# Optimization experiments

Measured on AMD Instinct MI355X. Metric: run time of the kernel, lower is better.

The kernel has to match this reference:

```python
import jax, jax.numpy as jnp
import numpy as np
from jax import lax

EPS = 1e-5
B, CIN, H, W = 4, 512, 64, 64
CI = CIN // 4          # inter_channels = 128
CQK = CI // 8          # PAM query/key channels = 16
NC = 19                # num_classes


def conv2d(x, w, pad):
    return lax.conv_general_dilated(x, w, (1, 1), [(pad, pad), (pad, pad)],
                                    dimension_numbers=('NCHW', 'OIHW', 'NCHW'))


def bn_relu(x, g, b, m, v):
    # eval-mode BatchNorm2d followed by ReLU
    inv = g * lax.rsqrt(v + EPS)
    return jax.nn.relu(x * inv[None, :, None, None] + (b - m * inv)[None, :, None, None])


def setup_inputs() -> dict:
    key = jax.random.key(0)
    ks = iter(jax.random.split(key, 40))
    rn = lambda shape, s=0.02: (jax.random.normal(next(ks), shape, dtype=jnp.float32) * s)
    ones = lambda n: jnp.ones((n,), jnp.float32)
    zeros = lambda n: jnp.zeros((n,), jnp.float32)
    inp = {
        'x': jax.random.normal(next(ks), (B, CIN, H, W), dtype=jnp.float32),
        # conv_p1: 3x3 conv (no bias) + BN
        'wp1': rn((CI, CIN, 3, 3)),
        'bnp1_w': ones(CI), 'bnp1_b': zeros(CI), 'bnp1_m': zeros(CI), 'bnp1_v': ones(CI),
        # PAM 1x1 convs
        'qw': rn((CQK, CI, 1, 1)), 'qb': zeros(CQK),
        'kw': rn((CQK, CI, 1, 1)), 'kb': zeros(CQK),
        'vw': rn((CI, CI, 1, 1)), 'vb': zeros(CI),
        'pam_gamma': jnp.full((1,), 0.5, jnp.float32),
        # conv_p2
        'wp2': rn((CI, CI, 3, 3)),
        'bnp2_w': ones(CI), 'bnp2_b': zeros(CI), 'bnp2_m': zeros(CI), 'bnp2_v': ones(CI),
        # conv_c1
        'wc1': rn((CI, CIN, 3, 3)),
        'bnc1_w': ones(CI), 'bnc1_b': zeros(CI), 'bnc1_m': zeros(CI), 'bnc1_v': ones(CI),
        'cam_gamma': jnp.full((1,), 0.5, jnp.float32),
        # conv_c2
        'wc2': rn((CI, CI, 3, 3)),
        'bnc2_w': ones(CI), 'bnc2_b': zeros(CI), 'bnc2_m': zeros(CI), 'bnc2_v': ones(CI),
        # classifier heads (dropout is eval-mode identity)
        'cls_w': rn((NC, CI, 1, 1)), 'cls_b': zeros(NC),
        'auxp_w': rn((NC, CI, 1, 1)), 'auxp_b': zeros(NC),
        'auxc_w': rn((NC, CI, 1, 1)), 'auxc_b': zeros(NC),
    }
    return inp


def pam(x, qw, qb, kw, kb, vw, vb, gamma):
    b, c, h, w = x.shape
    n = h * w
    q = (conv2d(x, qw, 0) + qb[None, :, None, None]).reshape(b, -1, n)  # [B,CQK,N]
    k = (conv2d(x, kw, 0) + kb[None, :, None, None]).reshape(b, -1, n)  # [B,CQK,N]
    v = (conv2d(x, vw, 0) + vb[None, :, None, None]).reshape(b, c, n)   # [B,C,N]
    attn = jax.nn.softmax(jnp.einsum('bcn,bcm->bnm', q, k), axis=-1)    # [B,N,N]
    out = jnp.einsum('bcm,bnm->bcn', v, attn).reshape(b, c, h, w)
    return gamma * out + x


def cam(x, gamma):
    b, c, h, w = x.shape
    f = x.reshape(b, c, -1)                                             # [B,C,N]
    attn = jax.nn.softmax(jnp.einsum('bin,bjn->bij', f, f), axis=-1)    # [B,C,C]
    out = jnp.einsum('bij,bjn->bin', attn, f).reshape(b, c, h, w)
    return gamma * out + x


def _forward(x, wp1, bnp1_w, bnp1_b, bnp1_m, bnp1_v,
             qw, qb, kw, kb, vw, vb, pam_gamma,
             wp2, bnp2_w, bnp2_b, bnp2_m, bnp2_v,
             wc1, bnc1_w, bnc1_b, bnc1_m, bnc1_v, cam_gamma,
             wc2, bnc2_w, bnc2_b, bnc2_m, bnc2_v,
             cls_w, cls_b, auxp_w, auxp_b, auxc_w, auxc_b):
    feat_p = bn_relu(conv2d(x, wp1, 1), bnp1_w, bnp1_b, bnp1_m, bnp1_v)
    feat_p = pam(feat_p, qw, qb, kw, kb, vw, vb, pam_gamma)
    feat_p = bn_relu(conv2d(feat_p, wp2, 1), bnp2_w, bnp2_b, bnp2_m, bnp2_v)

    feat_c = bn_relu(conv2d(x, wc1, 1), bnc1_w, bnc1_b, bnc1_m, bnc1_v)
    feat_c = cam(feat_c, cam_gamma)
    feat_c = bn_relu(conv2d(feat_c, wc2, 1), bnc2_w, bnc2_b, bnc2_m, bnc2_v)

    feat = feat_p + feat_c
    out = conv2d(feat, cls_w, 0) + cls_b[None, :, None, None]
    out_p = conv2d(feat_p, auxp_w, 0) + auxp_b[None, :, None, None]
    out_c = conv2d(feat_c, auxc_w, 0) + auxc_b[None, :, None, None]
    return out, out_p, out_c


def reference(x, wp1, bnp1_w, bnp1_b, bnp1_m, bnp1_v,
              qw, qb, kw, kb, vw, vb, pam_gamma,
              wp2, bnp2_w, bnp2_b, bnp2_m, bnp2_v,
              wc1, bnc1_w, bnc1_b, bnc1_m, bnc1_v, cam_gamma,
              wc2, bnc2_w, bnc2_b, bnc2_m, bnc2_v,
              cls_w, cls_b, auxp_w, auxp_b, auxc_w, auxc_b):
    return _forward(x, wp1, bnp1_w, bnp1_b, bnp1_m, bnp1_v,
                    qw, qb, kw, kb, vw, vb, pam_gamma,
                    wp2, bnp2_w, bnp2_b, bnp2_m, bnp2_v,
                    wc1, bnc1_w, bnc1_b, bnc1_m, bnc1_v, cam_gamma,
                    wc2, bnc2_w, bnc2_b, bnc2_m, bnc2_v,
                    cls_w, cls_b, auxp_w, auxp_b, auxc_w, auxc_b)
```

## Files before the change

### kernel.cpp

```cpp
#include <hip/hip_runtime.h>
#include <cstdint>
#include <cstddef>


using s16x8 = __attribute__((ext_vector_type(8))) short;
using u16x8 = __attribute__((ext_vector_type(8))) unsigned short;
using u16x4 = __attribute__((ext_vector_type(4))) unsigned short;
using f32x4 = __attribute__((ext_vector_type(4))) float;
using f32x16 = __attribute__((ext_vector_type(16))) float;
using u32x4v = __attribute__((ext_vector_type(4))) unsigned;

__device__ __forceinline__ f32x4 mfma16(u16x8 a, u16x8 b, f32x4 c) {
  return __builtin_amdgcn_mfma_f32_16x16x32_bf16(
      __builtin_bit_cast(s16x8, a), __builtin_bit_cast(s16x8, b), c, 0, 0, 0);
}
__device__ __forceinline__ f32x16 mfma32(u16x8 a, u16x8 b, f32x16 c) {
  return __builtin_amdgcn_mfma_f32_32x32x16_bf16(
      __builtin_bit_cast(s16x8, a), __builtin_bit_cast(s16x8, b), c, 0, 0, 0);
}
__device__ __forceinline__ float bf2f(unsigned short u) {
  return __builtin_bit_cast(float, (unsigned)u << 16);
}
__device__ __forceinline__ unsigned short f2bf(float f) {
  unsigned u = __builtin_bit_cast(unsigned, f);
  u += 0x7fffu + ((u >> 16) & 1u);
  return (unsigned short)(u >> 16);
}
__device__ __forceinline__ unsigned cvt_pk_bf16(float lo, float hi) {
  unsigned r;
  asm("v_cvt_pk_bf16_f32 %0, %1, %2" : "=v"(r) : "v"(lo), "v"(hi));
  return r;
}
__device__ __forceinline__ u16x8 ld8(const unsigned short* p) {
  return *reinterpret_cast<const u16x8*>(p);
}
__device__ __forceinline__ void gload16(const void* g, void* l) {
  __builtin_amdgcn_global_load_lds(
      (const __attribute__((address_space(1))) void*)g,
      (__attribute__((address_space(3))) void*)l, 16, 0, 0);
}

#define OFF_XT    ((size_t)0)
#define OFF_FP1   ((size_t)19464192)
#define OFF_FC1   ((size_t)24330240)
#define ZERO_BYTES ((size_t)29196288)
#define OFF_FP0   ((size_t)29196288)
#define OFF_FC0   ((size_t)33390592)
#define OFF_FP2   ((size_t)37584896)
#define OFF_FC2   ((size_t)41779200)
#define OFF_WT1   ((size_t)45973504)
#define OFF_WT2   ((size_t)48332800)
#define OFF_QKW   ((size_t)48922624)
#define OFF_VWW   ((size_t)48930816)
#define OFF_HWW   ((size_t)48963584)
#define OFF_BNSS  ((size_t)48988160)
#define OFF_ATTN  ((size_t)48992256)
#define OFF_Q     OFF_FP2
#define OFF_K     (OFF_FP2 + 524288)
#define OFF_V     OFF_FC2

__global__ __launch_bounds__(256) void k_xpose(const float* __restrict__ x,
                                               unsigned short* __restrict__ xt) {
  __shared__ float tile[128][65];
  const int t = threadIdx.x;
  const int blk = blockIdx.x;
  const int cb = blk & 3;
  const int h = (blk >> 2) & 63;
  const int b = blk >> 8;
  const float* src = x + ((size_t)(b * 512 + cb * 128) * 64 + h) * 64;
  const int w = t & 63, cr = t >> 6;
  for (int i = 0; i < 32; ++i) tile[cr + i * 4][w] = src[(size_t)(cr + i * 4) * 4096 + w];
  __syncthreads();
  const int w2 = t >> 2, cg = t & 3;
  const int cic = cb * 2 + (cg >> 1);
  unsigned short* dst =
      xt + (((size_t)(b * 8 + cic) * 66 + h + 1) * 72 + (w2 + 1)) * 64 + (cg & 1) * 32;
#pragma unroll
  for (int j = 0; j < 32; j += 4) {
    u16x4 pk;
    pk[0] = f2bf(tile[cg * 32 + j + 0][w2]);
    pk[1] = f2bf(tile[cg * 32 + j + 1][w2]);
    pk[2] = f2bf(tile[cg * 32 + j + 2][w2]);
    pk[3] = f2bf(tile[cg * 32 + j + 3][w2]);
    *reinterpret_cast<u16x4*>(dst + j) = pk;
  }
}

struct PackArgs {
  const float *wp1, *wc1, *wp2, *wc2, *qw, *kw, *vw, *clsw, *apw, *acw;
  const float *g1p, *b1p, *m1p, *v1p, *g1c, *b1c, *m1c, *v1c;
  const float *g2p, *b2p, *m2p, *v2p, *g2c, *b2c, *m2c, *v2c;
  unsigned short *wt1, *wt2, *qkw, *vww, *hww;
  float* bnss;
};
__global__ __launch_bounds__(256) void k_pack(PackArgs A) {
  const int i = blockIdx.x * 256 + threadIdx.x;
  const int N1 = 2 * 8 * 9 * 128 * 64;
  const int N2 = N1 + 2 * 2 * 9 * 128 * 64;
  const int N3 = N2 + 2 * 16 * 128;
  const int N4 = N3 + 128 * 128;
  const int N5 = N4 + 3 * 32 * 128;
  const int N6 = N5 + 8 * 128;
  if (i < N1) {
    int ci = i & 63, co = (i >> 6) & 127;
    int rest = i >> 13;
    int tap = rest % 9, cc = rest / 9;
    int cic = cc & 7, brr = cc >> 3;
    const float* s = brr ? A.wc1 : A.wp1;
    A.wt1[i] = f2bf(s[(size_t)(co * 512 + cic * 64 + ci) * 9 + tap]);
  } else if (i < N2) {
    int k = i - N1;
    int ci = k & 63, co = (k >> 6) & 127;
    int rest = k >> 13;
    int tap = rest % 9, cc = rest / 9;
    int cic = cc & 1, brr = cc >> 1;
    const float* s = brr ? A.wc2 : A.wp2;
    A.wt2[k] = f2bf(s[(size_t)(co * 128 + cic * 64 + ci) * 9 + tap]);
  } else if (i < N3) {
    int k = i - N2;
    int ci = k & 127, q = k >> 7;
    const float* s = (q < 16) ? A.qw : A.kw;
    A.qkw[k] = f2bf(s[(q & 15) * 128 + ci]);
  } else if (i < N4) {
    int k = i - N3;
    A.vww[k] = f2bf(A.vw[k]);
  } else if (i < N5) {
    int k = i - N4;
    int ci = k & 127, co = (k >> 7) & 31, hd = k >> 12;
    const float* s = hd == 0 ? A.clsw : (hd == 1 ? A.apw : A.acw);
    A.hww[k] = (co < 19) ? f2bf(s[co * 128 + ci]) : (unsigned short)0;
  } else if (i < N6) {
    int k = i - N5;
    int j = k & 127, seg = k >> 7;
    const float *g, *bb, *mm, *vv;
    switch (seg >> 1) {
      case 0: g = A.g1p; bb = A.b1p; mm = A.m1p; vv = A.v1p; break;
      case 1: g = A.g1c; bb = A.b1c; mm = A.m1c; vv = A.v1c; break;
      case 2: g = A.g2p; bb = A.b2p; mm = A.m2p; vv = A.v2p; break;
      default: g = A.g2c; bb = A.b2c; mm = A.m2c; vv = A.v2c; break;
    }
    float sc = g[j] * rsqrtf(vv[j] + 1e-5f);
    A.bnss[k] = (seg & 1) ? (bb[j] - mm[j] * sc) : sc;
  }
}

template <int NCHUNK>
__global__ __launch_bounds__(256) void k_conv3x3(
    const unsigned short* __restrict__ in0, const unsigned short* __restrict__ in1,
    const unsigned short* __restrict__ wt, const float* __restrict__ bnb,
    unsigned short* __restrict__ out0, unsigned short* __restrict__ out1) {
  __shared__ unsigned short Abuf[2][4 * 72 * 64];
  const int bid = blockIdx.x;
  const int ht = bid & 31;
  const int b = (bid >> 5) & 3;
  const int br = bid >> 7;
  const unsigned short* inp = br ? in1 : in0;
  const unsigned short* wbr = wt + (size_t)br * NCHUNK * 9 * 128 * 64;
  const float* scale = bnb + br * 256;
  const float* shiftp = scale + 128;
  unsigned short* outp = br ? out1 : out0;
  const int lane = threadIdx.x & 63, wv = threadIdx.x >> 6;
  const int lg = lane >> 4, l15 = lane & 15;
  const int wn = (wv & 1) * 64, cob = (wv >> 1) * 64;
  const int h0 = ht * 2;
  const int srow = h0 + wv;
  const int stoff = lane * 16;

  int hib[4];
  int swz[4][3];
#pragma unroll
  for (int mf = 0; mf < 4; ++mf) {
    int n = wn + mf * 16 + l15;
    int oh = n >> 6, w = n & 63;
    hib[mf] = (oh * 72 + w) * 128;
#pragma unroll
    for (int tx = 0; tx < 3; ++tx) swz[mf][tx] = ((w + tx) & 7) << 4;
  }
  const int lo16 = lg * 16;

  f32x4 acc[4][4];
#pragma unroll
  for (int mf = 0; mf < 4; ++mf)
#pragma unroll
    for (int nf = 0; nf < 4; ++nf) acc[mf][nf] = (f32x4){0.f, 0.f, 0.f, 0.f};

  auto stage = [&](int bi, int c) {
    const char* sr =
        (const char*)(inp + (((size_t)(b * NCHUNK + c) * 66 + srow) * 72) * 64);
    unsigned short* db = &Abuf[bi][wv * (72 * 64)];
#pragma unroll
    for (int i = 0; i < 9; ++i) {
      int d = i * 1024 + stoff;
      int sb = d ^ (((d >> 7) & 7) << 4);
      gload16(sr + sb, (void*)(db + i * 512));
    }
  };

  stage(0, 0);
#pragma unroll 1
  for (int c = 0; c < NCHUNK; ++c) {
    if (c + 1 < NCHUNK) {
      stage((c + 1) & 1, c + 1);
      asm volatile("s_waitcnt vmcnt(9) lgkmcnt(0)" ::: "memory");
    } else {
      asm volatile("s_waitcnt vmcnt(0) lgkmcnt(0)" ::: "memory");
    }
    __builtin_amdgcn_s_barrier();
    const unsigned short* wch = wbr + (size_t)c * (9 * 128 * 64);
    const char* ab = (const char*)(&Abuf[c & 1][0]);
#pragma unroll
    for (int ty = 0; ty < 3; ++ty)
#pragma unroll
      for (int tx = 0; tx < 3; ++tx) {
        const int tap = ty * 3 + tx;
        const unsigned short* wtap = wch + (size_t)tap * (128 * 64);
        const int rowoff = (ty * 72 + tx) * 128;
#pragma unroll
        for (int kc = 0; kc < 64; kc += 32) {
          u16x8 bv[4], av[4];
#pragma unroll
          for (int nf = 0; nf < 4; ++nf)
            bv[nf] = ld8(wtap + (size_t)(cob + nf * 16 + l15) * 64 + kc + lg * 8);
#pragma unroll
          for (int mf = 0; mf < 4; ++mf)
            av[mf] = *(const u16x8*)(ab + (hib[mf] + rowoff) +
                                     ((kc * 2 + lo16) ^ swz[mf][tx]));
#pragma unroll
          for (int mf = 0; mf < 4; ++mf)
#pragma unroll
            for (int nf = 0; nf < 4; ++nf)
              acc[mf][nf] = mfma16(av[mf], bv[nf], acc[mf][nf]);
        }
      }
    asm volatile("s_waitcnt lgkmcnt(0)" ::: "memory");
    __builtin_amdgcn_s_barrier();
  }
#pragma unroll
  for (int nf = 0; nf < 4; ++nf) {
    const int co = cob + nf * 16 + l15;
    const float sc = scale[co], sh = shiftp[co];
#pragma unroll
    for (int mf = 0; mf < 4; ++mf)
#pragma unroll
      for (int r = 0; r < 4; ++r) {
        int n = wn + mf * 16 + lg * 4 + r;
        float y = acc[mf][nf][r] * sc + sh;
        y = y > 0.f ? y : 0.f;
        outp[((size_t)b * 4096 + (size_t)(h0 + (n >> 6)) * 64 + (n & 63)) * 128 + co] =
            f2bf(y);
      }
  }
}

__global__ __launch_bounds__(256) void k_qkv(
    const unsigned short* __restrict__ fp0, const unsigned short* __restrict__ qkw,
    const unsigned short* __restrict__ vww, const float* __restrict__ qb,
    const float* __restrict__ kb, const float* __restrict__ vb,
    unsigned short* __restrict__ Q, unsigned short* __restrict__ K,
    unsigned short* __restrict__ V2) {
  const int bid = blockIdx.x;
  const int nt = bid & 63, b = bid >> 6;
  const int lane = threadIdx.x & 63, wv = threadIdx.x >> 6;
  const int lg = lane >> 4, l15 = lane & 15;
  const int n = nt * 64 + wv * 16 + l15;
  const unsigned short* fbase = fp0 + ((size_t)b * 4096 + n) * 128 + lg * 8;
  f32x4 vacc[8];
#pragma unroll
  for (int mf = 0; mf < 8; ++mf) vacc[mf] = (f32x4){0.f, 0.f, 0.f, 0.f};
  f32x4 qacc = {0.f, 0.f, 0.f, 0.f}, kacc = {0.f, 0.f, 0.f, 0.f};
#pragma unroll
  for (int kc = 0; kc < 128; kc += 32) {
    u16x8 fb = ld8(fbase + kc);
    u16x8 qa = ld8(qkw + (size_t)l15 * 128 + lg * 8 + kc);
    u16x8 ka = ld8(qkw + 2048 + (size_t)l15 * 128 + lg * 8 + kc);
    qacc = mfma16(qa, fb, qacc);
    kacc = mfma16(ka, fb, kacc);
#pragma unroll
    for (int mf = 0; mf < 8; ++mf) {
      u16x8 va = ld8(vww + (size_t)(mf * 16 + l15) * 128 + lg * 8 + kc);
      vacc[mf] = mfma16(va, fb, vacc[mf]);
    }
  }
  const float LOG2E = 1.44269504088896f;
#pragma unroll
  for (int r = 0; r < 4; ++r) {
    int cq = lg * 4 + r;
    Q[(size_t)(b * 4096 + n) * 16 + cq] = f2bf((qacc[r] + qb[cq]) * LOG2E);
    K[(size_t)(b * 4096 + n) * 16 + cq] = f2bf(kacc[r] + kb[cq]);
  }
#pragma unroll
  for (int mf = 0; mf < 8; ++mf)
#pragma unroll
    for (int r = 0; r < 4; ++r) {
      int c = mf * 16 + lg * 4 + r;
      V2[((size_t)(b * 512 + (n >> 3)) * 128 + c) * 8 + (n & 7)] =
          f2bf(vacc[mf][r] + vb[c]);
    }
}

__global__ __launch_bounds__(512, 1) void k_pam(
    const unsigned short* __restrict__ Q, const unsigned short* __restrict__ K,
    const unsigned short* __restrict__ V2, const unsigned short* __restrict__ fp0,
    unsigned short* __restrict__ fp1, const float* __restrict__ pg) {
  __shared__ float obuf[2][3][16][64][4];
  __shared__ float lred[8][64];
  const int bid = blockIdx.x;
  const int qt = bid & 63, b = bid >> 6;
  const int tid = threadIdx.x;
  const int lane = tid & 63, wv = tid >> 6;
  const int qsub = wv >> 2, mq = wv & 3;
  const int l31 = lane & 31, hi = lane >> 5;
  const int q0 = qt * 64 + qsub * 32;
  const unsigned short* Qp = Q + (size_t)b * 65536;
  const unsigned short* Kp = K + (size_t)b * 65536;
  const unsigned short* Vp = V2 + (size_t)b * 524288;
  const int hi8 = hi * 8;

  const u16x8 qB = ld8(Qp + (size_t)(q0 + l31) * 16 + hi8);

  f32x16 oacc[4];
#pragma unroll
  for (int ch = 0; ch < 4; ++ch) oacc[ch] = (f32x16)0.f;
  float dsum = 0.f;

  auto loadK = [&](int t) -> u16x8 {
    return ld8(Kp + (size_t)(t * 32 + l31) * 16 + hi8);
  };
  auto loadV = [&](int t, u16x8 (&vf)[8]) {
#pragma unroll
    for (int kc = 0; kc < 2; ++kc)
#pragma unroll
      for (int ch = 0; ch < 4; ++ch)
        vf[kc * 4 + ch] =
            ld8(Vp + (size_t)(t * 4 + kc * 2 + hi) * 1024 + (ch * 32 + l31) * 8);
  };
  auto body = [&](u16x8 kA, u16x8 (&vf)[8]) {
    f32x16 pacc = mfma32(kA, qB, (f32x16)0.f);
    float p[16];
#pragma unroll
    for (int r = 0; r < 16; ++r) p[r] = exp2f(pacc[r]);
    dsum += (((p[0] + p[1]) + (p[2] + p[3])) + ((p[4] + p[5]) + (p[6] + p[7]))) +
            (((p[8] + p[9]) + (p[10] + p[11])) + ((p[12] + p[13]) + (p[14] + p[15])));
    unsigned X[8], S[8];
#pragma unroll
    for (int j = 0; j < 8; ++j) X[j] = cvt_pk_bf16(p[2 * j], p[2 * j + 1]);
#pragma unroll
    for (int j = 0; j < 8; ++j) S[j] = __shfl_xor(X[j], 32, 64);
    const bool hc = hi != 0;
    u32x4v w0, w1;
    w0[0] = hc ? S[2] : X[0];
    w0[1] = hc ? S[3] : X[1];
    w0[2] = hc ? X[2] : S[0];
    w0[3] = hc ? X[3] : S[1];
    w1[0] = hc ? S[6] : X[4];
    w1[1] = hc ? S[7] : X[5];
    w1[2] = hc ? X[6] : S[4];
    w1[3] = hc ? X[7] : S[5];
    u16x8 f0 = __builtin_bit_cast(u16x8, w0);
    u16x8 f1 = __builtin_bit_cast(u16x8, w1);
#pragma unroll
    for (int ch = 0; ch < 4; ++ch) oacc[ch] = mfma32(f0, vf[ch], oacc[ch]);
#pragma unroll
    for (int ch = 0; ch < 4; ++ch) oacc[ch] = mfma32(f1, vf[4 + ch], oacc[ch]);
  };

  const int t0 = mq * 32;
  u16x8 kA0 = loadK(t0), kA1;
  u16x8 vf0[8], vf1[8];
  loadV(t0, vf0);
#pragma unroll 1
  for (int t = 0; t < 32; t += 2) {
    kA1 = loadK(t0 + t + 1);
    loadV(t0 + t + 1, vf1);
    body(kA0, vf0);
    if (t + 2 < 32) {
      kA0 = loadK(t0 + t + 2);
      loadV(t0 + t + 2, vf0);
    }
    body(kA1, vf1);
  }

  dsum += __shfl_xor(dsum, 32, 64);
  lred[wv][lane] = dsum;
  if (mq) {
#pragma unroll
    for (int ch = 0; ch < 4; ++ch)
#pragma unroll
      for (int j = 0; j < 4; ++j) {
        f32x4 v = {oacc[ch][4 * j + 0], oacc[ch][4 * j + 1], oacc[ch][4 * j + 2],
                   oacc[ch][4 * j + 3]};
        *reinterpret_cast<f32x4*>(&obuf[qsub][mq - 1][ch * 4 + j][lane][0]) = v;
      }
  }
  __syncthreads();
  if (mq == 0) {
    const float dtot = lred[qsub * 4 + 0][lane] + lred[qsub * 4 + 1][lane] +
                       lred[qsub * 4 + 2][lane] + lred[qsub * 4 + 3][lane];
#pragma unroll
    for (int ch = 0; ch < 4; ++ch)
#pragma unroll
      for (int j = 0; j < 4; ++j) {
        f32x4 s0 = *reinterpret_cast<const f32x4*>(&obuf[qsub][0][ch * 4 + j][lane][0]);
        f32x4 s1 = *reinterpret_cast<const f32x4*>(&obuf[qsub][1][ch * 4 + j][lane][0]);
        f32x4 s2 = *reinterpret_cast<const f32x4*>(&obuf[qsub][2][ch * 4 + j][lane][0]);
#pragma unroll
        for (int r = 0; r < 4; ++r)
          oacc[ch][4 * j + r] += (s0[r] + s1[r]) + s2[r];
      }
    const float rden = 1.f / dtot;
    const float gm = pg[0];
    float rdr[16];
#pragma unroll
    for (int r = 0; r < 16; ++r)
      rdr[r] = __shfl(rden, (r & 3) + 8 * (r >> 2) + 4 * hi, 64);
#pragma unroll
    for (int ch = 0; ch < 4; ++ch) {
      const int c = ch * 32 + l31;
#pragma unroll
      for (int r = 0; r < 16; ++r) {
        const int n = q0 + (r & 3) + 8 * (r >> 2) + 4 * hi;
        float o = gm * oacc[ch][r] * rdr[r] +
                  bf2f(fp0[((size_t)b * 4096 + n) * 128 + c]);
        fp1[(((size_t)(b * 2 + (c >> 6)) * 66 + (n >> 6) + 1) * 72 + ((n & 63) + 1)) *
                64 +
            (c & 63)] = f2bf(o);
      }
    }
  }
}

__global__ __launch_bounds__(256) void k_gram(const unsigned short* __restrict__ fc0,
                                              float* __restrict__ Gp) {
  __shared__ float fl[32][132];
  const int bid = blockIdx.x;
  const int nc = bid & 63, b = bid >> 6;
  const int t = threadIdx.x;
  const int i = t >> 1, jh = (t & 1) * 64;
  float acc[64];
#pragma unroll
  for (int j = 0; j < 64; ++j) acc[j] = 0.f;
  for (int c2 = 0; c2 < 2; ++c2) {
    const int n0 = nc * 64 + c2 * 32;
    {
      int nn = t >> 3, kh = t & 7;
      const unsigned short* src = fc0 + ((size_t)b * 4096 + n0 + nn) * 128 + kh * 16;
      u16x8 v0 = ld8(src), v1 = ld8(src + 8);
#pragma unroll
      for (int e = 0; e < 8; ++e) {
        fl[nn][kh * 16 + e] = bf2f(v0[e]);
        fl[nn][kh * 16 + 8 + e] = bf2f(v1[e]);
      }
    }
    __syncthreads();
    for (int nn = 0; nn < 32; ++nn) {
      float fi = fl[nn][i];
      const float4* row = reinterpret_cast<const float4*>(&fl[nn][jh]);
#pragma unroll
      for (int j4 = 0; j4 < 16; ++j4) {
        float4 fv = row[j4];
        acc[4 * j4 + 0] += fi * fv.x;
        acc[4 * j4 + 1] += fi * fv.y;
        acc[4 * j4 + 2] += fi * fv.z;
        acc[4 * j4 + 3] += fi * fv.w;
      }
    }
    __syncthreads();
  }
  float* dst = Gp + (((size_t)b * 64 + nc) * 128 + i) * 128 + jh;
  float4* dst4 = reinterpret_cast<float4*>(dst);
#pragma unroll
  for (int j4 = 0; j4 < 16; ++j4)
    dst4[j4] = make_float4(acc[4 * j4], acc[4 * j4 + 1], acc[4 * j4 + 2], acc[4 * j4 + 3]);
}

__global__ __launch_bounds__(128) void k_softm(const float* __restrict__ Gp,
                                               unsigned short* __restrict__ attn) {
  const int bid = blockIdx.x;
  const int i = bid & 127, b = bid >> 7;
  const int j = threadIdx.x;
  float g = 0.f;
  for (int nc = 0; nc < 64; ++nc) g += Gp[(((size_t)b * 64 + nc) * 128 + i) * 128 + j];
  __shared__ float red[2], red2[2];
  float m = g;
  m = fmaxf(m, __shfl_xor(m, 1, 64));
  m = fmaxf(m, __shfl_xor(m, 2, 64));
  m = fmaxf(m, __shfl_xor(m, 4, 64));
  m = fmaxf(m, __shfl_xor(m, 8, 64));
  m = fmaxf(m, __shfl_xor(m, 16, 64));
  m = fmaxf(m, __shfl_xor(m, 32, 64));
  const int wvi = j >> 6;
  if ((j & 63) == 0) red[wvi] = m;
  __syncthreads();
  m = fmaxf(red[0], red[1]);
  float e = __expf(g - m);
  float s = e;
  s += __shfl_xor(s, 1, 64);
  s += __shfl_xor(s, 2, 64);
  s += __shfl_xor(s, 4, 64);
  s += __shfl_xor(s, 8, 64);
  s += __shfl_xor(s, 16, 64);
  s += __shfl_xor(s, 32, 64);
  if ((j & 63) == 0) red2[wvi] = s;
  __syncthreads();
  s = red2[0] + red2[1];
  attn[((size_t)b * 128 + i) * 128 + j] = f2bf(e / s);
}

__global__ __launch_bounds__(256) void k_camout(
    const unsigned short* __restrict__ fc0, const unsigned short* __restrict__ attn,
    const float* __restrict__ cg, unsigned short* __restrict__ fc1) {
  const int bid = blockIdx.x;
  const int nt = bid & 63, b = bid >> 6;
  const int lane = threadIdx.x & 63, wv = threadIdx.x >> 6;
  const int lg = lane >> 4, l15 = lane & 15;
  const int n = nt * 64 + wv * 16 + l15;
  const unsigned short* fbase = fc0 + ((size_t)b * 4096 + n) * 128 + lg * 8;
  const unsigned short* abase = attn + (size_t)b * 16384 + lg * 8;
  f32x4 acc[8];
#pragma unroll
  for (int mf = 0; mf < 8; ++mf) acc[mf] = (f32x4){0.f, 0.f, 0.f, 0.f};
#pragma unroll
  for (int kc = 0; kc < 128; kc += 32) {
    u16x8 fb = ld8(fbase + kc);
#pragma unroll
    for (int mf = 0; mf < 8; ++mf) {
      u16x8 aa = ld8(abase + (size_t)(mf * 16 + l15) * 128 + kc);
      acc[mf] = mfma16(aa, fb, acc[mf]);
    }
  }
  const float gm = cg[0];
  const int nn = nt * 64 + wv * 16 + l15;
#pragma unroll
  for (int mf = 0; mf < 8; ++mf)
#pragma unroll
    for (int r = 0; r < 4; ++r) {
      int c = mf * 16 + lg * 4 + r;
      float o = gm * acc[mf][r] + bf2f(fc0[((size_t)b * 4096 + nn) * 128 + c]);
      fc1[(((size_t)(b * 2 + (c >> 6)) * 66 + (nn >> 6) + 1) * 72 + (nn & 63) + 1) * 64 +
          (c & 63)] = f2bf(o);
    }
}

__global__ __launch_bounds__(256) void k_heads(
    const unsigned short* __restrict__ fp2, const unsigned short* __restrict__ fc2,
    const unsigned short* __restrict__ hw, const float* __restrict__ clsb,
    const float* __restrict__ apb, const float* __restrict__ acb,
    float* __restrict__ out) {
  const int bid = blockIdx.x;
  const int nt = bid & 63, b = bid >> 6;
  const int lane = threadIdx.x & 63, wv = threadIdx.x >> 6;
  const int lg = lane >> 4, l15 = lane & 15;
  const int n = nt * 64 + wv * 16 + l15;
  const unsigned short* pb = fp2 + (size_t)(b * 4096 + n) * 128 + lg * 8;
  const unsigned short* cb = fc2 + (size_t)(b * 4096 + n) * 128 + lg * 8;
  f32x4 acc[3][2];
#pragma unroll
  for (int hd = 0; hd < 3; ++hd)
#pragma unroll
    for (int mf = 0; mf < 2; ++mf) acc[hd][mf] = (f32x4){0.f, 0.f, 0.f, 0.f};
#pragma unroll
  for (int kc = 0; kc < 128; kc += 32) {
    u16x8 vp = ld8(pb + kc);
    u16x8 vc = ld8(cb + kc);
    u16x8 vs;
#pragma unroll
    for (int e = 0; e < 8; ++e) vs[e] = f2bf(bf2f(vp[e]) + bf2f(vc[e]));
#pragma unroll
    for (int mf = 0; mf < 2; ++mf) {
      u16x8 a0 = ld8(hw + (size_t)(0 * 32 + mf * 16 + l15) * 128 + lg * 8 + kc);
      u16x8 a1 = ld8(hw + (size_t)(1 * 32 + mf * 16 + l15) * 128 + lg * 8 + kc);
      u16x8 a2 = ld8(hw + (size_t)(2 * 32 + mf * 16 + l15) * 128 + lg * 8 + kc);
      acc[0][mf] = mfma16(a0, vs, acc[0][mf]);
      acc[1][mf] = mfma16(a1, vp, acc[1][mf]);
      acc[2][mf] = mfma16(a2, vc, acc[2][mf]);
    }
  }
  const float* bias[3] = {clsb, apb, acb};
  const size_t hoff[3] = {0, 311296, 622592};
#pragma unroll
  for (int hd = 0; hd < 3; ++hd)
#pragma unroll
    for (int mf = 0; mf < 2; ++mf)
#pragma unroll
      for (int r = 0; r < 4; ++r) {
        int co = mf * 16 + lg * 4 + r;
        if (co < 19)
          out[hoff[hd] + ((size_t)b * 19 + co) * 4096 + n] = acc[hd][mf][r] + bias[hd][co];
      }
}

extern "C" void kernel_launch(void* const* d_in, const int* in_sizes, int n_in,
                              void* d_out, int out_size, void* d_ws, size_t ws_size,
                              hipStream_t stream) {
  (void)in_sizes; (void)n_in; (void)out_size; (void)ws_size;
  const float* x = (const float*)d_in[0];
  const float* wp1 = (const float*)d_in[1];
  const float* g1p = (const float*)d_in[2];
  const float* b1p = (const float*)d_in[3];
  const float* m1p = (const float*)d_in[4];
  const float* v1p = (const float*)d_in[5];
  const float* qw = (const float*)d_in[6];
  const float* qb = (const float*)d_in[7];
  const float* kw = (const float*)d_in[8];
  const float* kb = (const float*)d_in[9];
  const float* vw = (const float*)d_in[10];
  const float* vb = (const float*)d_in[11];
  const float* pamg = (const float*)d_in[12];
  const float* wp2 = (const float*)d_in[13];
  const float* g2p = (const float*)d_in[14];
  const float* b2p = (const float*)d_in[15];
  const float* m2p = (const float*)d_in[16];
  const float* v2p = (const float*)d_in[17];
  const float* wc1 = (const float*)d_in[18];
  const float* g1c = (const float*)d_in[19];
  const float* b1c = (const float*)d_in[20];
  const float* m1c = (const float*)d_in[21];
  const float* v1c = (const float*)d_in[22];
  const float* camg = (const float*)d_in[23];
  const float* wc2 = (const float*)d_in[24];
  const float* g2c = (const float*)d_in[25];
  const float* b2c = (const float*)d_in[26];
  const float* m2c = (const float*)d_in[27];
  const float* v2c = (const float*)d_in[28];
  const float* clsw = (const float*)d_in[29];
  const float* clsb = (const float*)d_in[30];
  const float* apw = (const float*)d_in[31];
  const float* apb = (const float*)d_in[32];
  const float* acw = (const float*)d_in[33];
  const float* acb = (const float*)d_in[34];

  char* ws = (char*)d_ws;
  unsigned short* xt = (unsigned short*)(ws + OFF_XT);
  unsigned short* fp1 = (unsigned short*)(ws + OFF_FP1);
  unsigned short* fc1 = (unsigned short*)(ws + OFF_FC1);
  unsigned short* fp0 = (unsigned short*)(ws + OFF_FP0);
  unsigned short* fc0 = (unsigned short*)(ws + OFF_FC0);
  unsigned short* fp2 = (unsigned short*)(ws + OFF_FP2);
  unsigned short* fc2 = (unsigned short*)(ws + OFF_FC2);
  unsigned short* wt1 = (unsigned short*)(ws + OFF_WT1);
  unsigned short* wt2 = (unsigned short*)(ws + OFF_WT2);
  unsigned short* qkw = (unsigned short*)(ws + OFF_QKW);
  unsigned short* vww = (unsigned short*)(ws + OFF_VWW);
  unsigned short* hww = (unsigned short*)(ws + OFF_HWW);
  float* bnss = (float*)(ws + OFF_BNSS);
  unsigned short* Qb = (unsigned short*)(ws + OFF_Q);
  unsigned short* Kb = (unsigned short*)(ws + OFF_K);
  unsigned short* Vb = (unsigned short*)(ws + OFF_V);
  unsigned short* attnb = (unsigned short*)(ws + OFF_ATTN);
  float* Gp = (float*)(ws + OFF_XT);

  hipMemsetAsync(ws, 0, ZERO_BYTES, stream);

  PackArgs pa;
  pa.wp1 = wp1; pa.wc1 = wc1; pa.wp2 = wp2; pa.wc2 = wc2;
  pa.qw = qw; pa.kw = kw; pa.vw = vw; pa.clsw = clsw; pa.apw = apw; pa.acw = acw;
  pa.g1p = g1p; pa.b1p = b1p; pa.m1p = m1p; pa.v1p = v1p;
  pa.g1c = g1c; pa.b1c = b1c; pa.m1c = m1c; pa.v1c = v1c;
  pa.g2p = g2p; pa.b2p = b2p; pa.m2p = m2p; pa.v2p = v2p;
  pa.g2c = g2c; pa.b2c = b2c; pa.m2c = m2c; pa.v2c = v2c;
  pa.wt1 = wt1; pa.wt2 = wt2; pa.qkw = qkw; pa.vww = vww; pa.hww = hww; pa.bnss = bnss;
  k_pack<<<5892, 256, 0, stream>>>(pa);

  k_xpose<<<1024, 256, 0, stream>>>(x, xt);

  k_conv3x3<8><<<256, 256, 0, stream>>>(xt, xt, wt1, bnss, fp0, fc0);

  k_qkv<<<256, 256, 0, stream>>>(fp0, qkw, vww, qb, kb, vb, Qb, Kb, Vb);
  k_gram<<<256, 256, 0, stream>>>(fc0, Gp);
  k_pam<<<256, 512, 0, stream>>>(Qb, Kb, Vb, fp0, fp1, pamg);
  k_softm<<<512, 128, 0, stream>>>(Gp, attnb);
  k_camout<<<256, 256, 0, stream>>>(fc0, attnb, camg, fc1);

  k_conv3x3<2><<<256, 256, 0, stream>>>(fp1, fc1, wt2, bnss + 512, fp2, fc2);

  k_heads<<<256, 256, 0, stream>>>(fp2, fc2, hww, clsb, apb, acb, (float*)d_out);
}
```

Measured before the change: 228.4 us.

## Use 8 waves per conv block with register-staged LDS double buffering

The 3x3 conv kernel now launches 512 threads per block, and each wave computes half as many output pixels. The first four waves stage input rows through registers into LDS, replacing the direct global-to-LDS loads, and they write the next chunk after computing the current one. The goal is more waves per CU to hide MFMA and memory latency, with the next load in flight during compute. The cost is that each wave now reloads weight fragments while getting half the pixel reuse, which doubles weight-load traffic per MFMA. The register staging also adds VGPR pressure and extra VALU/LDS write work.

```diff
diff --git a/kernel.cpp b/kernel.cpp
--- a/kernel.cpp
+++ b/kernel.cpp
@@ -33,11 +33,6 @@
 }
 __device__ __forceinline__ u16x8 ld8(const unsigned short* p) {
   return *reinterpret_cast<const u16x8*>(p);
-}
-__device__ __forceinline__ void gload16(const void* g, void* l) {
-  __builtin_amdgcn_global_load_lds(
-      (const __attribute__((address_space(1))) void*)g,
-      (__attribute__((address_space(3))) void*)l, 16, 0, 0);
 }
 
 #define OFF_XT    ((size_t)0)
@@ -145,7 +140,7 @@
 }
 
 template <int NCHUNK>
-__global__ __launch_bounds__(256) void k_conv3x3(
+__global__ __launch_bounds__(512, 2) void k_conv3x3(
     const unsigned short* __restrict__ in0, const unsigned short* __restrict__ in1,
     const unsigned short* __restrict__ wt, const float* __restrict__ bnb,
     unsigned short* __restrict__ out0, unsigned short* __restrict__ out1) {
@@ -161,51 +156,57 @@
   unsigned short* outp = br ? out1 : out0;
   const int lane = threadIdx.x & 63, wv = threadIdx.x >> 6;
   const int lg = lane >> 4, l15 = lane & 15;
-  const int wn = (wv & 1) * 64, cob = (wv >> 1) * 64;
+  const int nq = wv >> 1, ch = wv & 1;
+  const int wn = nq * 32, cob = ch * 64;
   const int h0 = ht * 2;
+  const bool stager = (wv < 4);
   const int srow = h0 + wv;
-  const int stoff = lane * 16;
-
-  int hib[4];
-  int swz[4][3];
-#pragma unroll
-  for (int mf = 0; mf < 4; ++mf) {
+
+  int hib[2];
+  int swz[2][3];
+#pragma unroll
+  for (int mf = 0; mf < 2; ++mf) {
     int n = wn + mf * 16 + l15;
     int oh = n >> 6, w = n & 63;
     hib[mf] = (oh * 72 + w) * 128;
 #pragma unroll
     for (int tx = 0; tx < 3; ++tx) swz[mf][tx] = ((w + tx) & 7) << 4;
   }
-  const int lo16 = lg * 16;
-
-  f32x4 acc[4][4];
-#pragma unroll
-  for (int mf = 0; mf < 4; ++mf)
+
+  f32x4 acc[2][4];
+#pragma unroll
+  for (int mf = 0; mf < 2; ++mf)
 #pragma unroll
     for (int nf = 0; nf < 4; ++nf) acc[mf][nf] = (f32x4){0.f, 0.f, 0.f, 0.f};
 
-  auto stage = [&](int bi, int c) {
+  u16x8 streg[9];
+  auto sload = [&](int c) {
     const char* sr =
         (const char*)(inp + (((size_t)(b * NCHUNK + c) * 66 + srow) * 72) * 64);
-    unsigned short* db = &Abuf[bi][wv * (72 * 64)];
 #pragma unroll
     for (int i = 0; i < 9; ++i) {
-      int d = i * 1024 + stoff;
+      int d = i * 1024 + lane * 16;
       int sb = d ^ (((d >> 7) & 7) << 4);
-      gload16(sr + sb, (void*)(db + i * 512));
+      streg[i] = *(const u16x8*)(sr + sb);
     }
   };
-
-  stage(0, 0);
+  auto swrite = [&](int bi) {
+    char* db = (char*)&Abuf[bi][wv * (72 * 64)];
+#pragma unroll
+    for (int i = 0; i < 9; ++i)
+      *(u16x8*)(db + i * 1024 + lane * 16) = streg[i];
+  };
+
+  if (stager) sload(0);
+  asm volatile("s_waitcnt vmcnt(0)" ::: "memory");
+  if (stager) swrite(0);
+  asm volatile("s_waitcnt lgkmcnt(0)" ::: "memory");
+  __builtin_amdgcn_s_barrier();
+
 #pragma unroll 1
   for (int c = 0; c < NCHUNK; ++c) {
-    if (c + 1 < NCHUNK) {
-      stage((c + 1) & 1, c + 1);
-      asm volatile("s_waitcnt vmcnt(9) lgkmcnt(0)" ::: "memory");
-    } else {
-      asm volatile("s_waitcnt vmcnt(0) lgkmcnt(0)" ::: "memory");
-    }
-    __builtin_amdgcn_s_barrier();
+    if (stager && c + 1 < NCHUNK) sload(c + 1);
+    asm volatile("" ::: "memory");
     const unsigned short* wch = wbr + (size_t)c * (9 * 128 * 64);
     const char* ab = (const char*)(&Abuf[c & 1][0]);
 #pragma unroll
@@ -217,30 +218,35 @@
         const int rowoff = (ty * 72 + tx) * 128;
 #pragma unroll
         for (int kc = 0; kc < 64; kc += 32) {
-          u16x8 bv[4], av[4];
+          u16x8 bv[4], av[2];
 #pragma unroll
           for (int nf = 0; nf < 4; ++nf)
             bv[nf] = ld8(wtap + (size_t)(cob + nf * 16 + l15) * 64 + kc + lg * 8);
 #pragma unroll
-          for (int mf = 0; mf < 4; ++mf)
+          for (int mf = 0; mf < 2; ++mf)
             av[mf] = *(const u16x8*)(ab + (hib[mf] + rowoff) +
-                                     ((kc * 2 + lo16) ^ swz[mf][tx]));
-#pragma unroll
-          for (int mf = 0; mf < 4; ++mf)
+                                     ((kc * 2 + lg * 16) ^ swz[mf][tx]));
+#pragma unroll
+          for (int mf = 0; mf < 2; ++mf)
 #pragma unroll
             for (int nf = 0; nf < 4; ++nf)
               acc[mf][nf] = mfma16(av[mf], bv[nf], acc[mf][nf]);
         }
       }
+    if (c + 1 < NCHUNK) {
+      asm volatile("s_waitcnt vmcnt(0)" ::: "memory");
+      if (stager) swrite((c + 1) & 1);
+    }
     asm volatile("s_waitcnt lgkmcnt(0)" ::: "memory");
     __builtin_amdgcn_s_barrier();
   }
+
 #pragma unroll
   for (int nf = 0; nf < 4; ++nf) {
     const int co = cob + nf * 16 + l15;
     const float sc = scale[co], sh = shiftp[co];
 #pragma unroll
-    for (int mf = 0; mf < 4; ++mf)
+    for (int mf = 0; mf < 2; ++mf)
 #pragma unroll
       for (int r = 0; r < 4; ++r) {
         int n = wn + mf * 16 + lg * 4 + r;
@@ -663,7 +669,7 @@
 
   k_xpose<<<1024, 256, 0, stream>>>(x, xt);
 
-  k_conv3x3<8><<<256, 256, 0, stream>>>(xt, xt, wt1, bnss, fp0, fc0);
+  k_conv3x3<8><<<256, 512, 0, stream>>>(xt, xt, wt1, bnss, fp0, fc0);
 
   k_qkv<<<256, 256, 0, stream>>>(fp0, qkw, vww, qb, kb, vb, Qb, Kb, Vb);
   k_gram<<<256, 256, 0, stream>>>(fc0, Gp);
@@ -671,7 +677,7 @@
   k_softm<<<512, 128, 0, stream>>>(Gp, attnb);
   k_camout<<<256, 256, 0, stream>>>(fc0, attnb, camg, fc1);
 
-  k_conv3x3<2><<<256, 256, 0, stream>>>(fp1, fc1, wt2, bnss + 512, fp2, fc2);
+  k_conv3x3<2><<<256, 512, 0, stream>>>(fp1, fc1, wt2, bnss + 512, fp2, fc2);
 
   k_heads<<<256, 256, 0, stream>>>(fp2, fc2, hww, clsb, apb, acb, (float*)d_out);
 }
```

Measured after the change: 305.6 us. 1.34x slower.

## Stage conv3x3 weights in LDS, use 32x32 MFMA, pre-swizzle producer layouts

Applied to the files above, without the earlier changes.

The 3x3 conv kernel now double-buffers per-tap-row weight tiles in shared memory through async global-to-LDS loads. Previously each wave read its weights straight from global memory. The input window is prefetched into registers and written to LDS once per chunk. The MFMA shape moves from 16x16x32 to 32x32x16, with a 2x2 fragment tile per wave. Because of this, the producer kernels (transpose, pack, PAM/CAM outputs) now write their data pre-XOR-swizzled so plain copies land bank-conflict-free. The cost is more LDS use, one block per CU via launch bounds, and extra barriers.

```diff
diff --git a/kernel.cpp b/kernel.cpp
--- a/kernel.cpp
+++ b/kernel.cpp
@@ -73,15 +73,17 @@
   __syncthreads();
   const int w2 = t >> 2, cg = t & 3;
   const int cic = cb * 2 + (cg >> 1);
+  const int kk = ((w2 + 1) & 7) << 3;
   unsigned short* dst =
       xt + (((size_t)(b * 8 + cic) * 66 + h + 1) * 72 + (w2 + 1)) * 64 + (cg & 1) * 32;
 #pragma unroll
   for (int j = 0; j < 32; j += 4) {
+    const int sb = (cg >> 1) * 64 + (((cg & 1) * 32 + j) ^ kk);
     u16x4 pk;
-    pk[0] = f2bf(tile[cg * 32 + j + 0][w2]);
-    pk[1] = f2bf(tile[cg * 32 + j + 1][w2]);
-    pk[2] = f2bf(tile[cg * 32 + j + 2][w2]);
-    pk[3] = f2bf(tile[cg * 32 + j + 3][w2]);
+    pk[0] = f2bf(tile[sb + 0][w2]);
+    pk[1] = f2bf(tile[sb + 1][w2]);
+    pk[2] = f2bf(tile[sb + 2][w2]);
+    pk[3] = f2bf(tile[sb + 3][w2]);
     *reinterpret_cast<u16x4*>(dst + j) = pk;
   }
 }
@@ -107,7 +109,8 @@
     int tap = rest % 9, cc = rest / 9;
     int cic = cc & 7, brr = cc >> 3;
     const float* s = brr ? A.wc1 : A.wp1;
-    A.wt1[i] = f2bf(s[(size_t)(co * 512 + cic * 64 + ci) * 9 + tap]);
+    int cis = ci ^ ((co & 7) << 3);
+    A.wt1[i] = f2bf(s[(size_t)(co * 512 + cic * 64 + cis) * 9 + tap]);
   } else if (i < N2) {
     int k = i - N1;
     int ci = k & 63, co = (k >> 6) & 127;
@@ -115,7 +118,8 @@
     int tap = rest % 9, cc = rest / 9;
     int cic = cc & 1, brr = cc >> 1;
     const float* s = brr ? A.wc2 : A.wp2;
-    A.wt2[k] = f2bf(s[(size_t)(co * 128 + cic * 64 + ci) * 9 + tap]);
+    int cis = ci ^ ((co & 7) << 3);
+    A.wt2[k] = f2bf(s[(size_t)(co * 128 + cic * 64 + cis) * 9 + tap]);
   } else if (i < N3) {
     int k = i - N2;
     int ci = k & 127, q = k >> 7;
@@ -145,11 +149,12 @@
 }
 
 template <int NCHUNK>
-__global__ __launch_bounds__(256) void k_conv3x3(
+__global__ __launch_bounds__(256, 1) void k_conv3x3(
     const unsigned short* __restrict__ in0, const unsigned short* __restrict__ in1,
     const unsigned short* __restrict__ wt, const float* __restrict__ bnb,
     unsigned short* __restrict__ out0, unsigned short* __restrict__ out1) {
-  __shared__ unsigned short Abuf[2][4 * 72 * 64];
+  __shared__ unsigned short Awin[4 * 72 * 64];
+  __shared__ unsigned short Wbuf[2][3 * 128 * 64];
   const int bid = blockIdx.x;
   const int ht = bid & 31;
   const int b = (bid >> 5) & 3;
@@ -159,91 +164,132 @@
   const float* scale = bnb + br * 256;
   const float* shiftp = scale + 128;
   unsigned short* outp = br ? out1 : out0;
-  const int lane = threadIdx.x & 63, wv = threadIdx.x >> 6;
-  const int lg = lane >> 4, l15 = lane & 15;
-  const int wn = (wv & 1) * 64, cob = (wv >> 1) * 64;
+  const int tid = threadIdx.x;
+  const int lane = tid & 63, wv = tid >> 6;
+  const int l31 = lane & 31, hi = lane >> 5;
+  const int hi16 = hi * 16;
+  const int nq = wv & 1, ch = wv >> 1;
+  const int wn = nq * 64, cob = ch * 64;
   const int h0 = ht * 2;
-  const int srow = h0 + wv;
-  const int stoff = lane * 16;
-
-  int hib[4];
-  int swz[4][3];
-#pragma unroll
-  for (int mf = 0; mf < 4; ++mf) {
-    int n = wn + mf * 16 + l15;
-    int oh = n >> 6, w = n & 63;
-    hib[mf] = (oh * 72 + w) * 128;
-#pragma unroll
-    for (int tx = 0; tx < 3; ++tx) swz[mf][tx] = ((w + tx) & 7) << 4;
-  }
-  const int lo16 = lg * 16;
-
-  f32x4 acc[4][4];
-#pragma unroll
-  for (int mf = 0; mf < 4; ++mf)
-#pragma unroll
-    for (int nf = 0; nf < 4; ++nf) acc[mf][nf] = (f32x4){0.f, 0.f, 0.f, 0.f};
-
-  auto stage = [&](int bi, int c) {
+
+  int aw[2], arow[2];
+#pragma unroll
+  for (int mf = 0; mf < 2; ++mf) {
+    int n = wn + mf * 32 + l31;
+    aw[mf] = n & 63;
+    arow[mf] = (n >> 6) * 72;
+  }
+  int bvbase[2];
+#pragma unroll
+  for (int nf = 0; nf < 2; ++nf) bvbase[nf] = (cob + nf * 32 + l31) * 128;
+  const int bkey = (l31 & 7) << 4;
+
+  f32x16 acc[2][2];
+#pragma unroll
+  for (int mf = 0; mf < 2; ++mf)
+#pragma unroll
+    for (int nf = 0; nf < 2; ++nf) acc[mf][nf] = (f32x16)0.f;
+
+  u16x8 streg[9];
+  auto sloadA = [&](int c) {
     const char* sr =
-        (const char*)(inp + (((size_t)(b * NCHUNK + c) * 66 + srow) * 72) * 64);
-    unsigned short* db = &Abuf[bi][wv * (72 * 64)];
-#pragma unroll
-    for (int i = 0; i < 9; ++i) {
-      int d = i * 1024 + stoff;
-      int sb = d ^ (((d >> 7) & 7) << 4);
-      gload16(sr + sb, (void*)(db + i * 512));
-    }
+        (const char*)(inp + (((size_t)(b * NCHUNK + c) * 66 + h0) * 72) * 64);
+#pragma unroll
+    for (int i = 0; i < 9; ++i)
+      streg[i] = *(const u16x8*)(sr + i * 4096 + tid * 16);
   };
-
-  stage(0, 0);
+  auto swriteA = [&]() {
+    char* dp = (char*)Awin;
+#pragma unroll
+    for (int i = 0; i < 9; ++i)
+      *(u16x8*)(dp + i * 4096 + tid * 16) = streg[i];
+  };
+  auto stageW = [&](int bi, int T) {
+    const char* src = (const char*)wbr + (size_t)T * 49152;
+    char* dst = (char*)&Wbuf[bi][0];
+#pragma unroll
+    for (int i = 0; i < 12; ++i)
+      gload16(src + i * 4096 + tid * 16, dst + i * 4096 + tid * 16);
+  };
+
+  auto compute = [&](int g, int bi) {
+    const char* ab = (const char*)Awin;
+    const char* wb = (const char*)&Wbuf[bi][0];
+#pragma unroll
+    for (int tl = 0; tl < 3; ++tl) {
+      int abase[2], akey[2];
+#pragma unroll
+      for (int mf = 0; mf < 2; ++mf) {
+        int wc = aw[mf] + tl;
+        abase[mf] = ((arow[mf] + g * 72 + wc) << 7);
+        akey[mf] = (wc & 7) << 4;
+      }
+      const int wtl = tl << 14;
+#pragma unroll
+      for (int s = 0; s < 4; ++s) {
+        const int ko = s * 32 + hi16;
+        u16x8 av[2], bv[2];
+#pragma unroll
+        for (int mf = 0; mf < 2; ++mf)
+          av[mf] = *(const u16x8*)(ab + abase[mf] + (ko ^ akey[mf]));
+#pragma unroll
+        for (int nf = 0; nf < 2; ++nf)
+          bv[nf] = *(const u16x8*)(wb + wtl + bvbase[nf] + (ko ^ bkey));
+#pragma unroll
+        for (int mf = 0; mf < 2; ++mf)
+#pragma unroll
+          for (int nf = 0; nf < 2; ++nf)
+            acc[mf][nf] = mfma32(av[mf], bv[nf], acc[mf][nf]);
+      }
+    }
+  };
+
+  const int total = 3 * NCHUNK;
+  sloadA(0);
+  stageW(0, 0);
+  swriteA();
+  stageW(1, 1);
+  asm volatile("s_waitcnt vmcnt(12) lgkmcnt(0)\ns_barrier" ::: "memory");
+  if (NCHUNK > 1) sloadA(1);
+
 #pragma unroll 1
   for (int c = 0; c < NCHUNK; ++c) {
-    if (c + 1 < NCHUNK) {
-      stage((c + 1) & 1, c + 1);
-      asm volatile("s_waitcnt vmcnt(9) lgkmcnt(0)" ::: "memory");
-    } else {
-      asm volatile("s_waitcnt vmcnt(0) lgkmcnt(0)" ::: "memory");
-    }
-    __builtin_amdgcn_s_barrier();
-    const unsigned short* wch = wbr + (size_t)c * (9 * 128 * 64);
-    const char* ab = (const char*)(&Abuf[c & 1][0]);
-#pragma unroll
-    for (int ty = 0; ty < 3; ++ty)
-#pragma unroll
-      for (int tx = 0; tx < 3; ++tx) {
-        const int tap = ty * 3 + tx;
-        const unsigned short* wtap = wch + (size_t)tap * (128 * 64);
-        const int rowoff = (ty * 72 + tx) * 128;
-#pragma unroll
-        for (int kc = 0; kc < 64; kc += 32) {
-          u16x8 bv[4], av[4];
-#pragma unroll
-          for (int nf = 0; nf < 4; ++nf)
-            bv[nf] = ld8(wtap + (size_t)(cob + nf * 16 + l15) * 64 + kc + lg * 8);
-#pragma unroll
-          for (int mf = 0; mf < 4; ++mf)
-            av[mf] = *(const u16x8*)(ab + (hib[mf] + rowoff) +
-                                     ((kc * 2 + lo16) ^ swz[mf][tx]));
-#pragma unroll
-          for (int mf = 0; mf < 4; ++mf)
-#pragma unroll
-            for (int nf = 0; nf < 4; ++nf)
-              acc[mf][nf] = mfma16(av[mf], bv[nf], acc[mf][nf]);
+#pragma unroll
+    for (int g = 0; g < 3; ++g) {
+      const int T = c * 3 + g;
+      compute(g, T & 1);
+      if (T + 1 < total) {
+        asm volatile("s_waitcnt lgkmcnt(0)\ns_barrier" ::: "memory");
+        bool issuedA = false;
+        if (g == 2) {
+          swriteA();
+          if (c + 2 < NCHUNK) {
+            sloadA(c + 2);
+            issuedA = true;
+          }
         }
-      }
-    asm volatile("s_waitcnt lgkmcnt(0)" ::: "memory");
-    __builtin_amdgcn_s_barrier();
-  }
-#pragma unroll
-  for (int nf = 0; nf < 4; ++nf) {
-    const int co = cob + nf * 16 + l15;
+        if (T + 2 < total) {
+          stageW((T + 2) & 1, T + 2);
+          if (issuedA)
+            asm volatile("s_waitcnt vmcnt(21) lgkmcnt(0)\ns_barrier" ::: "memory");
+          else
+            asm volatile("s_waitcnt vmcnt(12) lgkmcnt(0)\ns_barrier" ::: "memory");
+        } else {
+          asm volatile("s_waitcnt vmcnt(0) lgkmcnt(0)\ns_barrier" ::: "memory");
+        }
+      }
+    }
+  }
+
+#pragma unroll
+  for (int nf = 0; nf < 2; ++nf) {
+    const int co = cob + nf * 32 + l31;
     const float sc = scale[co], sh = shiftp[co];
 #pragma unroll
-    for (int mf = 0; mf < 4; ++mf)
-#pragma unroll
-      for (int r = 0; r < 4; ++r) {
-        int n = wn + mf * 16 + lg * 4 + r;
+    for (int mf = 0; mf < 2; ++mf)
+#pragma unroll
+      for (int r = 0; r < 16; ++r) {
+        int n = wn + mf * 32 + (r & 3) + 8 * (r >> 2) + 4 * hi;
         float y = acc[mf][nf][r] * sc + sh;
         y = y > 0.f ? y : 0.f;
         outp[((size_t)b * 4096 + (size_t)(h0 + (n >> 6)) * 64 + (n & 63)) * 128 + co] =
@@ -419,11 +465,11 @@
 #pragma unroll
       for (int r = 0; r < 16; ++r) {
         const int n = q0 + (r & 3) + 8 * (r >> 2) + 4 * hi;
+        const int wp = (n & 63) + 1;
         float o = gm * oacc[ch][r] * rdr[r] +
                   bf2f(fp0[((size_t)b * 4096 + n) * 128 + c]);
-        fp1[(((size_t)(b * 2 + (c >> 6)) * 66 + (n >> 6) + 1) * 72 + ((n & 63) + 1)) *
-                64 +
-            (c & 63)] = f2bf(o);
+        fp1[(((size_t)(b * 2 + (c >> 6)) * 66 + (n >> 6) + 1) * 72 + wp) * 64 +
+            ((c & 63) ^ ((wp & 7) << 3))] = f2bf(o);
       }
     }
   }
@@ -530,14 +576,15 @@
   }
   const float gm = cg[0];
   const int nn = nt * 64 + wv * 16 + l15;
+  const int wp = (nn & 63) + 1;
 #pragma unroll
   for (int mf = 0; mf < 8; ++mf)
 #pragma unroll
     for (int r = 0; r < 4; ++r) {
       int c = mf * 16 + lg * 4 + r;
       float o = gm * acc[mf][r] + bf2f(fc0[((size_t)b * 4096 + nn) * 128 + c]);
-      fc1[(((size_t)(b * 2 + (c >> 6)) * 66 + (nn >> 6) + 1) * 72 + (nn & 63) + 1) * 64 +
-          (c & 63)] = f2bf(o);
+      fc1[(((size_t)(b * 2 + (c >> 6)) * 66 + (nn >> 6) + 1) * 72 + wp) * 64 +
+          ((c & 63) ^ ((wp & 7) << 3))] = f2bf(o);
     }
 }
 
```

After: 197.2 us. 13.6% less time.
